# Kernel tuning notes

Measured on AMD Instinct MI355X. Metric: run time of the kernel, lower is better.

Reference implementation:

```python
import jax, jax.numpy as jnp
import numpy as np

N = 100000   # nodes
E = 1600000  # edges per relation (avg in-degree 16)
D = 128      # gcn_hidden (in_feat == out_feat)
R = 2        # relations: forward_edge, backward_edge


def setup_inputs() -> dict:
    key = jax.random.key(0)
    ks = jax.random.split(key, 8)
    x = jax.random.normal(ks[0], (N, D), dtype=jnp.float32)
    src_fwd = jax.random.randint(ks[1], (E,), 0, N, dtype=jnp.int32)
    dst_fwd = jax.random.randint(ks[2], (E,), 0, N, dtype=jnp.int32)
    src_bwd = jax.random.randint(ks[3], (E,), 0, N, dtype=jnp.int32)
    dst_bwd = jax.random.randint(ks[4], (E,), 0, N, dtype=jnp.int32)
    # xavier_uniform with relu gain sqrt(2)
    gain = np.sqrt(2.0)
    lim_rel = gain * np.sqrt(6.0 / (D + D))
    rel_weight = jax.random.uniform(ks[5], (R, D, D), minval=-lim_rel, maxval=lim_rel, dtype=jnp.float32)
    loop_weight = jax.random.uniform(ks[6], (D, D), minval=-lim_rel, maxval=lim_rel, dtype=jnp.float32)
    h_bias = jnp.zeros((D,), dtype=jnp.float32)
    return {
        'x': x,
        'src_fwd': src_fwd, 'dst_fwd': dst_fwd,
        'src_bwd': src_bwd, 'dst_bwd': dst_bwd,
        'rel_weight': rel_weight, 'loop_weight': loop_weight, 'h_bias': h_bias,
    }


def _rel_conv(x, src, dst, W):
    # dgl GraphConv(norm='right', weight per relation): scatter-sum src feats to
    # dst, divide by clamped in-degree, then matmul W (in_feat == out_feat so
    # order of matmul vs aggregation is mathematically equivalent).
    msg = x[src]                                            # [E, D] gather
    agg = jax.ops.segment_sum(msg, dst, num_segments=N)     # [N, D] scatter-add
    deg = jax.ops.segment_sum(jnp.ones((src.shape[0],), x.dtype), dst, num_segments=N)
    agg = agg / jnp.clip(deg, 1.0)[:, None]                 # right norm, deg clamp(min=1)
    return agg @ W                                          # [N, D]


def reference(x, src_fwd, dst_fwd, src_bwd, dst_bwd, rel_weight, loop_weight, h_bias):
    h = _rel_conv(x, src_fwd, dst_fwd, rel_weight[0])
    h = h + _rel_conv(x, src_bwd, dst_bwd, rel_weight[1])   # HeteroGraphConv sums per-relation results
    h = h + x @ loop_weight                                 # self loop
    h = h + h_bias                                          # bias
    h = jax.nn.relu(h)                                      # activation
    return h                                                # dropout is identity in eval
```

## Files before the change

### kernel.cpp

```cpp
#include <hip/hip_runtime.h>
#include <hip/hip_bf16.h>


#define DFEAT 128
#define CH2 16384
#define NBMAX 1600
#define CAPN 2816

typedef __attribute__((ext_vector_type(8))) short short8v;
typedef __attribute__((ext_vector_type(4))) float float4v;
typedef __attribute__((ext_vector_type(2))) unsigned int uint2v;
typedef __attribute__((ext_vector_type(4))) unsigned short ushort4v;

__device__ __forceinline__ float4v bfexp(uint2v g) {
    float4v v;
    v[0] = __uint_as_float(g[0] << 16);
    v[1] = __uint_as_float(g[0] & 0xffff0000u);
    v[2] = __uint_as_float(g[1] << 16);
    v[3] = __uint_as_float(g[1] & 0xffff0000u);
    return v;
}

__global__ void pack_b_kernel(const float* __restrict__ wrel,
                              const float* __restrict__ wloop,
                              unsigned short* __restrict__ wb,
                              int* __restrict__ ghist, int NB) {
    int t = blockIdx.x * blockDim.x + threadIdx.x;
    if (t < NB) ghist[t] = 0;
    if (t >= 12 * 8 * 64) return;
    int lane = t & 63;
    int kbase = (t >> 9) * 32 + (lane >> 4) * 8;
    int col = (((t >> 6) & 7) << 4) + (lane & 15);
    unsigned short tmp[8];
#pragma unroll
    for (int j = 0; j < 8; ++j) {
        int k = kbase + j;
        float v = (k < 256) ? wrel[k * DFEAT + col] : wloop[(k - 256) * DFEAT + col];
        tmp[j] = __hip_bfloat16_raw(__float2bfloat16(v)).x;
    }
    *(ushort4*)(wb + t * 8)     = make_ushort4(tmp[0], tmp[1], tmp[2], tmp[3]);
    *(ushort4*)(wb + t * 8 + 4) = make_ushort4(tmp[4], tmp[5], tmp[6], tmp[7]);
}

__global__ __launch_bounds__(256) void conv_hist_kernel(
        const float4v* __restrict__ x4, ushort4v* __restrict__ xb4, int n4,
        const int* __restrict__ dst0, const int* __restrict__ dst1,
        int* __restrict__ ghist, int N, int E, int NB, int nhb) {
    if ((int)blockIdx.x < nhb) {
        __shared__ int h[NBMAX];
        int tid = threadIdx.x;
        for (int i = tid; i < NBMAX; i += 256) h[i] = 0;
        __syncthreads();
        int lo = blockIdx.x * CH2, hi = min(2 * E, lo + CH2);
        for (int i = lo + tid; i < hi; i += 256) {
            int r = (i >= E) ? 1 : 0;
            int e = i - r * E;
            int t = r ? dst1[e] : dst0[e];
            atomicAdd(&h[(r * N + t) >> 7], 1);
        }
        __syncthreads();
        for (int b = tid; b < NB; b += 256) {
            int c = h[b];
            if (c) atomicAdd(&ghist[b], c);
        }
    } else {
        int i = ((int)blockIdx.x - nhb) * 256 + threadIdx.x;
        if (i < n4) {
            float4v v = __builtin_nontemporal_load(x4 + i);
            ushort4v o;
            o[0] = __hip_bfloat16_raw(__float2bfloat16(v[0])).x;
            o[1] = __hip_bfloat16_raw(__float2bfloat16(v[1])).x;
            o[2] = __hip_bfloat16_raw(__float2bfloat16(v[2])).x;
            o[3] = __hip_bfloat16_raw(__float2bfloat16(v[3])).x;
            xb4[i] = o;
        }
    }
}

__global__ __launch_bounds__(256) void scan_kernel(const int* __restrict__ ghist,
                                                   int* __restrict__ S,
                                                   int* __restrict__ cursor,
                                                   int n, int total) {
    __shared__ int psum[256];
    int t = threadIdx.x;
    int cs = (n + 255) / 256;
    int s = 0;
    for (int j = 0; j < cs; ++j) {
        int idx = t * cs + j;
        if (idx < n) s += ghist[idx];
    }
    psum[t] = s; __syncthreads();
    for (int off = 1; off < 256; off <<= 1) {
        int add = (t >= off) ? psum[t - off] : 0;
        __syncthreads();
        psum[t] += add;
        __syncthreads();
    }
    int run = psum[t] - s;
    for (int j = 0; j < cs; ++j) {
        int idx = t * cs + j;
        if (idx < n) { S[idx] = run; cursor[idx] = run; run += ghist[idx]; }
    }
    if (t == 0) S[n] = total;
}

__global__ __launch_bounds__(256) void bin_kernel(
        const int* __restrict__ src0, const int* __restrict__ dst0,
        const int* __restrict__ src1, const int* __restrict__ dst1,
        int* __restrict__ cursor, unsigned* __restrict__ binned, int N, int E) {
    __shared__ int cnt[NBMAX];
    __shared__ int base[NBMAX];
    int tid = threadIdx.x;
    for (int i = tid; i < NBMAX; i += 256) cnt[i] = 0;
    __syncthreads();
    int lo = blockIdx.x * CH2, hi = min(2 * E, lo + CH2);
    for (int i = lo + tid; i < hi; i += 256) {
        int r = (i >= E) ? 1 : 0;
        int e = i - r * E;
        int t = r ? dst1[e] : dst0[e];
        atomicAdd(&cnt[(r * N + t) >> 7], 1);
    }
    __syncthreads();
    for (int b = tid; b < NBMAX; b += 256) {
        int c = cnt[b];
        if (c) base[b] = atomicAdd(&cursor[b], c);
    }
    __syncthreads();
    for (int i = lo + tid; i < hi; i += 256) {
        int r = (i >= E) ? 1 : 0;
        int e = i - r * E;
        int s = r ? src1[e] : src0[e];
        int t = r ? dst1[e] : dst0[e];
        int p = r * N + t;
        int slot = atomicAdd(&base[p >> 7], 1);
        binned[slot] = ((unsigned)(p & 127) << 17) | (unsigned)s;
    }
}

__global__ __launch_bounds__(256) void agg_kernel(
        const uint2v* __restrict__ xb2,
        const unsigned* __restrict__ binned,
        const int* __restrict__ S,
        unsigned short* __restrict__ aggb, int M) {
    __shared__ unsigned ebA[CAPN];
    __shared__ unsigned ebB[CAPN];
    __shared__ int cnt[128], cur[128], rs[128], sh[128];
    int tid = threadIdx.x;
    int b = blockIdx.x;
    int estart = S[b], eend = S[b + 1];
    int total = eend - estart;
    int P0 = b << 7;
    int hw = tid >> 5, lane = tid & 31;

    if (total <= CAPN) {
        if (tid < 128) cnt[tid] = 0;
        for (int i = tid; i < total; i += 256)
            ebA[i] = __builtin_nontemporal_load(binned + estart + i);
        __syncthreads();
        for (int i = tid; i < total; i += 256)
            atomicAdd(&cnt[ebA[i] >> 17], 1);
        __syncthreads();
        if (tid < 128) sh[tid] = cnt[tid];
        __syncthreads();
        for (int off = 1; off < 128; off <<= 1) {
            int add = (tid < 128 && tid >= off) ? sh[tid - off] : 0;
            __syncthreads();
            if (tid < 128) sh[tid] += add;
            __syncthreads();
        }
        if (tid < 128) { rs[tid] = sh[tid] - cnt[tid]; cur[tid] = sh[tid] - cnt[tid]; }
        __syncthreads();
        for (int i = tid; i < total; i += 256) {
            unsigned v = ebA[i];
            int slot = atomicAdd(&cur[v >> 17], 1);
            ebB[slot] = v;
        }
        __syncthreads();

        for (int pi = 0; pi < 16; ++pi) {
            int pl = hw * 16 + pi;
            int s0 = rs[pl], c = cnt[pl];
            float4v a = (float4v){0.f, 0.f, 0.f, 0.f};
            int e = 0;
            if (c >= 4) {
                int sA = ebB[s0]     & 0x1FFFF;
                int sB = ebB[s0 + 1] & 0x1FFFF;
                int sC = ebB[s0 + 2] & 0x1FFFF;
                int sD = ebB[s0 + 3] & 0x1FFFF;
                uint2v cAq = xb2[(size_t)sA * 32 + lane];
                uint2v cBq = xb2[(size_t)sB * 32 + lane];
                uint2v cCq = xb2[(size_t)sC * 32 + lane];
                uint2v cDq = xb2[(size_t)sD * 32 + lane];
                for (e = 4; e + 4 <= c; e += 4) {
                    int nA = ebB[s0 + e]     & 0x1FFFF;
                    int nB = ebB[s0 + e + 1] & 0x1FFFF;
                    int nC = ebB[s0 + e + 2] & 0x1FFFF;
                    int nD = ebB[s0 + e + 3] & 0x1FFFF;
                    uint2v gA = xb2[(size_t)nA * 32 + lane];
                    uint2v gB = xb2[(size_t)nB * 32 + lane];
                    uint2v gC = xb2[(size_t)nC * 32 + lane];
                    uint2v gD = xb2[(size_t)nD * 32 + lane];
                    float4v t0 = bfexp(cAq) + bfexp(cBq);
                    float4v t1 = bfexp(cCq) + bfexp(cDq);
                    a += t0 + t1;
                    cAq = gA; cBq = gB; cCq = gC; cDq = gD;
                }
                float4v t0 = bfexp(cAq) + bfexp(cBq);
                float4v t1 = bfexp(cCq) + bfexp(cDq);
                a += t0 + t1;
            }
            for (; e < c; ++e) {
                int s = ebB[s0 + e] & 0x1FFFF;
                a += bfexp(xb2[(size_t)s * 32 + lane]);
            }
            int pg = P0 + pl;
            if (pg < M) {
                float inv = 1.0f / (float)max(c, 1);
                ushort4v w;
                w[0] = __hip_bfloat16_raw(__float2bfloat16(a[0] * inv)).x;
                w[1] = __hip_bfloat16_raw(__float2bfloat16(a[1] * inv)).x;
                w[2] = __hip_bfloat16_raw(__float2bfloat16(a[2] * inv)).x;
                w[3] = __hip_bfloat16_raw(__float2bfloat16(a[3] * inv)).x;
                __builtin_nontemporal_store(
                    w, (ushort4v*)(aggb + (size_t)pg * DFEAT + 4 * lane));
            }
        }
    } else {
        for (int pi = 0; pi < 16; ++pi) {
            int pl = hw * 16 + pi;
            float4v a = (float4v){0.f, 0.f, 0.f, 0.f};
            int c = 0;
            for (int i = estart; i < eend; ++i) {
                unsigned v = binned[i];
                if ((int)(v >> 17) == pl) {
                    ++c;
                    a += bfexp(xb2[(size_t)(v & 0x1FFFF) * 32 + lane]);
                }
            }
            int pg = P0 + pl;
            if (pg < M) {
                float inv = 1.0f / (float)max(c, 1);
                ushort4v w;
                w[0] = __hip_bfloat16_raw(__float2bfloat16(a[0] * inv)).x;
                w[1] = __hip_bfloat16_raw(__float2bfloat16(a[1] * inv)).x;
                w[2] = __hip_bfloat16_raw(__float2bfloat16(a[2] * inv)).x;
                w[3] = __hip_bfloat16_raw(__float2bfloat16(a[3] * inv)).x;
                *(ushort4v*)(aggb + (size_t)pg * DFEAT + 4 * lane) = w;
            }
        }
    }
}

__global__ __launch_bounds__(256) void mfma_gemm_kernel(
        const unsigned short* __restrict__ aggb,
        const unsigned short* __restrict__ xb,
        const unsigned short* __restrict__ wb,
        const float* __restrict__ bias,
        float* __restrict__ out, int N) {
    int tid = threadIdx.x;
    int wv = tid >> 6, lane = tid & 63;
    int R0 = blockIdx.x * 128 + wv * 32;
    int mrow = lane & 15, quad = lane >> 4;

    float4v acc[2][8];
#pragma unroll
    for (int rt = 0; rt < 2; ++rt)
#pragma unroll
        for (int ct = 0; ct < 8; ++ct) acc[rt][ct] = (float4v){0.f, 0.f, 0.f, 0.f};

    int n0 = min(R0 + mrow, N - 1);
    int n1 = min(R0 + 16 + mrow, N - 1);

#pragma unroll
    for (int kc = 0; kc < 12; ++kc) {
        int off = (kc & 3) * 32 + quad * 8;
        const unsigned short* s0;
        const unsigned short* s1;
        if (kc < 4)      { s0 = aggb + (size_t)n0 * DFEAT;       s1 = aggb + (size_t)n1 * DFEAT; }
        else if (kc < 8) { s0 = aggb + (size_t)(N + n0) * DFEAT; s1 = aggb + (size_t)(N + n1) * DFEAT; }
        else             { s0 = xb + (size_t)n0 * DFEAT;         s1 = xb + (size_t)n1 * DFEAT; }
        short8v a0 = *(const short8v*)(s0 + off);
        short8v a1 = *(const short8v*)(s1 + off);
#pragma unroll
        for (int ct = 0; ct < 8; ++ct) {
            short8v bfr = *(const short8v*)(wb + (((kc * 8 + ct) << 6) + lane) * 8);
            acc[0][ct] = __builtin_amdgcn_mfma_f32_16x16x32_bf16(a0, bfr, acc[0][ct], 0, 0, 0);
            acc[1][ct] = __builtin_amdgcn_mfma_f32_16x16x32_bf16(a1, bfr, acc[1][ct], 0, 0, 0);
        }
    }

#pragma unroll
    for (int ct = 0; ct < 8; ++ct) {
        int col = ct * 16 + mrow;
        float bv = bias[col];
#pragma unroll
        for (int rt = 0; rt < 2; ++rt) {
#pragma unroll
            for (int i = 0; i < 4; ++i) {
                int row = R0 + rt * 16 + quad * 4 + i;
                if (row < N)
                    __builtin_nontemporal_store(fmaxf(acc[rt][ct][i] + bv, 0.f),
                                                out + (size_t)row * DFEAT + col);
            }
        }
    }
}

extern "C" void kernel_launch(void* const* d_in, const int* in_sizes, int n_in,
                              void* d_out, int out_size, void* d_ws, size_t ws_size,
                              hipStream_t stream) {
    const float* x      = (const float*)d_in[0];
    const int* src_fwd  = (const int*)d_in[1];
    const int* dst_fwd  = (const int*)d_in[2];
    const int* src_bwd  = (const int*)d_in[3];
    const int* dst_bwd  = (const int*)d_in[4];
    const float* wrel   = (const float*)d_in[5];
    const float* wloop  = (const float*)d_in[6];
    const float* hbias  = (const float*)d_in[7];
    float* out          = (float*)d_out;

    int N = in_sizes[0] / DFEAT;
    int E = in_sizes[1];
    int M = 2 * N;
    int TE = 2 * E;
    int NB = (M + 127) / 128;

    unsigned short* wb   = (unsigned short*)d_ws;
    unsigned* binned     = (unsigned*)(wb + 12 * 8 * 64 * 8);
    unsigned short* xb   = (unsigned short*)(binned + (size_t)TE);
    unsigned short* aggb = xb + (size_t)N * DFEAT;
    int* ghist           = (int*)(aggb + (size_t)M * DFEAT);
    int* S               = ghist + NB;
    int* cursor          = S + NB + 1;

    int n4 = N * (DFEAT / 4);
    int nconv = (n4 + 255) / 256;
    int nhb = (TE + CH2 - 1) / CH2;

    pack_b_kernel<<<24, 256, 0, stream>>>(wrel, wloop, wb, ghist, NB);

    conv_hist_kernel<<<nhb + nconv, 256, 0, stream>>>(
        (const float4v*)x, (ushort4v*)xb, n4, dst_fwd, dst_bwd, ghist, N, E, NB, nhb);

    scan_kernel<<<1, 256, 0, stream>>>(ghist, S, cursor, NB, TE);

    bin_kernel<<<nhb, 256, 0, stream>>>(
        src_fwd, dst_fwd, src_bwd, dst_bwd, cursor, binned, N, E);

    agg_kernel<<<NB, 256, 0, stream>>>((const uint2v*)xb, binned, S, aggb, M);

    mfma_gemm_kernel<<<(N + 127) / 128, 256, 0, stream>>>(
        aggb, xb, wb, hbias, out, N);
}
```

Measured before the change: 403.3 us.

## Halve destination bin size to 64 rows and slim aggregation shared memory

Destination bins shrink from 128 to 64 rows, so twice as many aggregation blocks launch, each using far less shared memory (one edge buffer instead of two). The block scan becomes a wavefront shuffle scan in place of a barrier-heavy shared-memory scan, and edges are read straight from global memory twice instead of being staged first. The aim is higher occupancy and fewer barriers during the gather-heavy aggregation. The costs are a larger histogram in the binning kernels, global edge reads done twice, and a tighter per-bin capacity that could push more bins onto the slow fallback path.

```diff
diff --git a/kernel.cpp b/kernel.cpp
--- a/kernel.cpp
+++ b/kernel.cpp
@@ -4,8 +4,9 @@
 
 #define DFEAT 128
 #define CH2 16384
-#define NBMAX 1600
-#define CAPN 2816
+#define PSH 6
+#define NBMAX 3200
+#define CAPN 1536
 
 typedef __attribute__((ext_vector_type(8))) short short8v;
 typedef __attribute__((ext_vector_type(4))) float float4v;
@@ -56,7 +57,7 @@
             int r = (i >= E) ? 1 : 0;
             int e = i - r * E;
             int t = r ? dst1[e] : dst0[e];
-            atomicAdd(&h[(r * N + t) >> 7], 1);
+            atomicAdd(&h[(r * N + t) >> PSH], 1);
         }
         __syncthreads();
         for (int b = tid; b < NB; b += 256) {
@@ -118,7 +119,7 @@
         int r = (i >= E) ? 1 : 0;
         int e = i - r * E;
         int t = r ? dst1[e] : dst0[e];
-        atomicAdd(&cnt[(r * N + t) >> 7], 1);
+        atomicAdd(&cnt[(r * N + t) >> PSH], 1);
     }
     __syncthreads();
     for (int b = tid; b < NBMAX; b += 256) {
@@ -132,8 +133,8 @@
         int s = r ? src1[e] : src0[e];
         int t = r ? dst1[e] : dst0[e];
         int p = r * N + t;
-        int slot = atomicAdd(&base[p >> 7], 1);
-        binned[slot] = ((unsigned)(p & 127) << 17) | (unsigned)s;
+        int slot = atomicAdd(&base[p >> PSH], 1);
+        binned[slot] = ((unsigned)(p & 63) << 17) | (unsigned)s;
     }
 }
 
@@ -142,60 +143,59 @@
         const unsigned* __restrict__ binned,
         const int* __restrict__ S,
         unsigned short* __restrict__ aggb, int M) {
-    __shared__ unsigned ebA[CAPN];
-    __shared__ unsigned ebB[CAPN];
-    __shared__ int cnt[128], cur[128], rs[128], sh[128];
+    __shared__ unsigned ebuf[CAPN];
+    __shared__ int cnt[64], cur[64], rs[64];
     int tid = threadIdx.x;
     int b = blockIdx.x;
     int estart = S[b], eend = S[b + 1];
     int total = eend - estart;
-    int P0 = b << 7;
+    int P0 = b << PSH;
     int hw = tid >> 5, lane = tid & 31;
 
     if (total <= CAPN) {
-        if (tid < 128) cnt[tid] = 0;
-        for (int i = tid; i < total; i += 256)
-            ebA[i] = __builtin_nontemporal_load(binned + estart + i);
-        __syncthreads();
-        for (int i = tid; i < total; i += 256)
-            atomicAdd(&cnt[ebA[i] >> 17], 1);
-        __syncthreads();
-        if (tid < 128) sh[tid] = cnt[tid];
-        __syncthreads();
-        for (int off = 1; off < 128; off <<= 1) {
-            int add = (tid < 128 && tid >= off) ? sh[tid - off] : 0;
-            __syncthreads();
-            if (tid < 128) sh[tid] += add;
-            __syncthreads();
-        }
-        if (tid < 128) { rs[tid] = sh[tid] - cnt[tid]; cur[tid] = sh[tid] - cnt[tid]; }
-        __syncthreads();
-        for (int i = tid; i < total; i += 256) {
-            unsigned v = ebA[i];
+        if (tid < 64) cnt[tid] = 0;
+        __syncthreads();
+        for (int i = estart + tid; i < eend; i += 256)
+            atomicAdd(&cnt[binned[i] >> 17], 1);
+        __syncthreads();
+        if (tid < 64) {
+            int v = cnt[tid];
+            int inc = v;
+#pragma unroll
+            for (int off = 1; off < 64; off <<= 1) {
+                int t2 = __shfl_up(inc, off);
+                if (tid >= off) inc += t2;
+            }
+            rs[tid] = inc - v;
+            cur[tid] = inc - v;
+        }
+        __syncthreads();
+        for (int i = estart + tid; i < eend; i += 256) {
+            unsigned v = binned[i];
             int slot = atomicAdd(&cur[v >> 17], 1);
-            ebB[slot] = v;
-        }
-        __syncthreads();
-
-        for (int pi = 0; pi < 16; ++pi) {
-            int pl = hw * 16 + pi;
+            ebuf[slot] = v;
+        }
+        __syncthreads();
+
+        for (int pi = 0; pi < 8; ++pi) {
+            int pl = hw * 8 + pi;
             int s0 = rs[pl], c = cnt[pl];
             float4v a = (float4v){0.f, 0.f, 0.f, 0.f};
             int e = 0;
             if (c >= 4) {
-                int sA = ebB[s0]     & 0x1FFFF;
-                int sB = ebB[s0 + 1] & 0x1FFFF;
-                int sC = ebB[s0 + 2] & 0x1FFFF;
-                int sD = ebB[s0 + 3] & 0x1FFFF;
+                int sA = ebuf[s0]     & 0x1FFFF;
+                int sB = ebuf[s0 + 1] & 0x1FFFF;
+                int sC = ebuf[s0 + 2] & 0x1FFFF;
+                int sD = ebuf[s0 + 3] & 0x1FFFF;
                 uint2v cAq = xb2[(size_t)sA * 32 + lane];
                 uint2v cBq = xb2[(size_t)sB * 32 + lane];
                 uint2v cCq = xb2[(size_t)sC * 32 + lane];
                 uint2v cDq = xb2[(size_t)sD * 32 + lane];
                 for (e = 4; e + 4 <= c; e += 4) {
-                    int nA = ebB[s0 + e]     & 0x1FFFF;
-                    int nB = ebB[s0 + e + 1] & 0x1FFFF;
-                    int nC = ebB[s0 + e + 2] & 0x1FFFF;
-                    int nD = ebB[s0 + e + 3] & 0x1FFFF;
+                    int nA = ebuf[s0 + e]     & 0x1FFFF;
+                    int nB = ebuf[s0 + e + 1] & 0x1FFFF;
+                    int nC = ebuf[s0 + e + 2] & 0x1FFFF;
+                    int nD = ebuf[s0 + e + 3] & 0x1FFFF;
                     uint2v gA = xb2[(size_t)nA * 32 + lane];
                     uint2v gB = xb2[(size_t)nB * 32 + lane];
                     uint2v gC = xb2[(size_t)nC * 32 + lane];
@@ -210,7 +210,7 @@
                 a += t0 + t1;
             }
             for (; e < c; ++e) {
-                int s = ebB[s0 + e] & 0x1FFFF;
+                int s = ebuf[s0 + e] & 0x1FFFF;
                 a += bfexp(xb2[(size_t)s * 32 + lane]);
             }
             int pg = P0 + pl;
@@ -226,8 +226,8 @@
             }
         }
     } else {
-        for (int pi = 0; pi < 16; ++pi) {
-            int pl = hw * 16 + pi;
+        for (int pi = 0; pi < 8; ++pi) {
+            int pl = hw * 8 + pi;
             float4v a = (float4v){0.f, 0.f, 0.f, 0.f};
             int c = 0;
             for (int i = estart; i < eend; ++i) {
@@ -323,7 +323,7 @@
     int E = in_sizes[1];
     int M = 2 * N;
     int TE = 2 * E;
-    int NB = (M + 127) / 128;
+    int NB = (M + 63) / 64;
 
     unsigned short* wb   = (unsigned short*)d_ws;
     unsigned* binned     = (unsigned*)(wb + 12 * 8 * 64 * 8);
```

Result: faster. 389.6 us (-3.4%).
